# Performance work log

Measured on AMD Instinct MI355X. Metric: run time of the kernel, lower is better.

## Reference

```python
import jax, jax.numpy as jnp
import numpy as np

C = 64
N_H = 4
N_WIN = 16
WIN_L = 8   # compressor window length (overlapped)
WIN_S = 4   # compressor stride -> T//4 blocks


def _rms(x, eps=1e-6):
    return x * jax.lax.rsqrt(jnp.mean(x * x, axis=-1, keepdims=True) + eps)


def _rope(x, negate=False):
    # x: (..., L, D); rotate-half RoPE over positions 0..L-1
    L, D = x.shape[-2], x.shape[-1]
    half = D // 2
    inv_freq = 1.0 / (10000.0 ** (jnp.arange(half, dtype=x.dtype) / half))
    ang = jnp.arange(L, dtype=x.dtype)[:, None] * inv_freq  # (L, half)
    if negate:
        ang = -ang
    cos, sin = jnp.cos(ang), jnp.sin(ang)
    x1, x2 = x[..., :half], x[..., half:]
    return jnp.concatenate([x1 * cos - x2 * sin, x1 * sin + x2 * cos], axis=-1)


def _compress(H, W):
    # overlapped token compressor: windows of WIN_L, stride WIN_S, zero-pad tail
    B, T, d = H.shape
    Tc = T // WIN_S
    Hp = jnp.pad(H, ((0, 0), (0, WIN_L - WIN_S), (0, 0)))
    idx = WIN_S * jnp.arange(Tc)[:, None] + jnp.arange(WIN_L)[None, :]  # (Tc, WIN_L)
    win = Hp[:, idx]                       # (B, Tc, WIN_L, d)
    return win.reshape(B, Tc, WIN_L * d) @ W  # (B, Tc, out)


def setup_inputs() -> dict:
    key = jax.random.key(0)
    ks = jax.random.split(key, 11)
    B, T, d = 2, 2048, 256

    def w(k, shape, fan):
        return jax.random.normal(k, shape, jnp.float32) / np.float32(np.sqrt(fan))

    H = jax.random.normal(ks[0], (B, T, d), jnp.float32)
    return {
        'H': H,
        'Wc_comp': w(ks[1], (WIN_L * d, C), WIN_L * d),
        'Wc_idx': w(ks[2], (WIN_L * d, 32), WIN_L * d),
        'W_DQ': w(ks[3], (d, 64), d),
        'W_IUQ': w(ks[4], (64, 4 * 32), 64),
        'W_w': w(ks[5], (64, 4), 64),
        'W_Q': w(ks[6], (d, N_H * C), d),
        'W_KV': w(ks[7], (d, C), d),
        'g_q': jnp.ones((N_H, C), jnp.float32),
        'g_k': jnp.ones((C,), jnp.float32),
        'g_v': jnp.ones((C,), jnp.float32),
        'Wg0': w(ks[8], (2 * C, 64), 2 * C),
        'bg0': jnp.zeros((64,), jnp.float32),
        'Wg1': w(ks[9], (2 * C, 64), 2 * C),
        'bg1': jnp.zeros((64,), jnp.float32),
        'Wout': w(ks[10], (128, d), 128),
        'bout': jnp.zeros((d,), jnp.float32),
    }


def reference(H, Wc_comp, Wc_idx, W_DQ, W_IUQ, W_w, W_Q, W_KV,
              g_q, g_k, g_v, Wg0, bg0, Wg1, bg1, Wout, bout):
    B, T, d = H.shape
    Tc = T // 4
    k_top = min(8, Tc)

    # ---- lightning indexer ----
    H_dc = H @ W_DQ                                   # (B,T,64)
    Q_I = (H_dc @ W_IUQ).reshape(B, T, 4, 32)         # (B,T,4,32)
    W_Iw = (H_dc @ W_w)[..., None]                    # (B,T,4,1)
    K_I = _compress(H, Wc_idx)                        # (B,Tc,32)
    dot = jnp.einsum('bthc,bsc->bths', Q_I, K_I)      # (B,T,4,Tc)
    I_ts = (W_Iw * jax.nn.relu(dot)).sum(axis=2)      # (B,T,Tc)

    t = jnp.arange(T)[:, None]
    s = jnp.arange(Tc)[None, :]
    mask_I = jnp.where(4 * s <= t, 0.0, -jnp.inf)     # (T,Tc) causal over blocks
    _, topk_idx = jax.lax.top_k(I_ts + mask_I, k_top)  # (B,T,k)
    bI = jnp.arange(B)[:, None, None]
    tI = jnp.arange(T)[None, :, None]
    M_comp = jnp.full((B, T, Tc), -jnp.inf).at[bI, tI, topk_idx].set(0.0)

    # ---- compressed + sliding KV ----
    KV = jnp.concatenate([_compress(H, Wc_comp), H @ W_KV], axis=1)  # (B,Tc+T,C)

    Q = (H @ W_Q).reshape(B, T, N_H, C).transpose(0, 2, 1, 3)        # (B,nh,T,C)
    Q = _rms(Q) * g_q[None, :, None, :]
    K = _rms(KV) * g_k
    V = _rms(KV) * g_v
    Q = _rope(Q)
    K = _rope(K)
    V = _rope(V)

    S = jnp.einsum('bhtc,bsc->bhts', Q, K) / np.float32(np.sqrt(C))  # (B,nh,T,Tc+T)

    S_comp = S[..., :Tc] + M_comp[:, None]
    rel = t - jnp.arange(T)[None, :]
    mask_slide = jnp.where((rel >= 0) & (rel < N_WIN), 0.0, -jnp.inf)  # (T,T)
    S_slide = S[..., Tc:] + mask_slide

    P = jax.nn.softmax(jnp.concatenate([S_comp, S_slide], axis=-1), axis=-1)
    O = jnp.einsum('bhts,bsc->bhtc', P, V)            # (B,nh,T,C)
    O = _rope(O, negate=True)

    O0 = O[:, :2].transpose(0, 2, 1, 3).reshape(B, T, 2 * C)
    O1 = O[:, 2:].transpose(0, 2, 1, 3).reshape(B, T, 2 * C)
    p_all = jnp.concatenate([O0 @ Wg0 + bg0, O1 @ Wg1 + bg1], axis=-1)
    return p_all @ Wout + bout
```

## Files before the change

kernel.cpp:

```cpp
#include <hip/hip_runtime.h>
#include <hip/hip_bf16.h>
#include <math.h>

#define T_DIM 2048
#define B_DIM 2
#define D_DIM 256
#define TC 512
#define KV_LEN 2560

typedef __attribute__((ext_vector_type(8))) short bf16x8;
typedef __attribute__((ext_vector_type(4))) float f32x4;
typedef unsigned short ush;

__device__ __forceinline__ float wave_sum64(float v) {
#pragma unroll
    for (int off = 32; off > 0; off >>= 1) v += __shfl_xor(v, off, 64);
    return v;
}

__device__ __forceinline__ float rope_angle(int pos, int j) {
    float inv = powf(10000.0f, -(float)j * (1.0f / 32.0f));
    return (float)pos * inv;
}

__global__ __launch_bounds__(256) void k_prep(
    const float* __restrict__ H, const float* __restrict__ W_Q,
    const float* __restrict__ W_KV, const float* __restrict__ W_DQ,
    const float* __restrict__ W_IUQ, const float* __restrict__ W_w,
    const float* __restrict__ Wc_comp, const float* __restrict__ Wc_idx,
    const float* __restrict__ Wg0, const float* __restrict__ bg0,
    const float* __restrict__ Wg1, const float* __restrict__ bg1,
    const float* __restrict__ Wout, const float* __restrict__ bout,
    ush* __restrict__ Ap, ush* __restrict__ Ac,
    ush* __restrict__ Bp, ush* __restrict__ Bc,
    ush* __restrict__ Bo, float* __restrict__ biascomb)
{
    int gid = blockIdx.x * 256 + threadIdx.x;
    float vals[8];
    ush* dst;
    bool lo_part;

    if (gid < 262144) {
        int tile = gid >> 10;
        int c = (gid >> 6) & 15;
        int l = gid & 63;
        int bt = tile * 16 + (l & 15);
        int kb = (c & 7) * 32 + (l >> 4) * 8;
        const float* src = H + (size_t)bt * 256 + kb;
#pragma unroll
        for (int j = 0; j < 8; ++j) vals[j] = src[j];
        lo_part = (c >= 8);
        dst = Ap + (size_t)gid * 8;
    } else if (gid < 786432) {
        int g = gid - 262144;
        int tile = g >> 13;
        int c = (g >> 6) & 127;
        int l = g & 63;
        int m = tile * 16 + (l & 15);
        int s = m & 511;
        int b = m >> 9;
        int k2b = (c & 63) * 32 + (l >> 4) * 8;
        int r4 = 4 * s + (k2b >> 8);
        int col = k2b & 255;
        if (r4 < T_DIM) {
            const float* src = H + ((size_t)b * T_DIM + r4) * 256 + col;
#pragma unroll
            for (int j = 0; j < 8; ++j) vals[j] = src[j];
        } else {
#pragma unroll
            for (int j = 0; j < 8; ++j) vals[j] = 0.f;
        }
        lo_part = (c >= 64);
        dst = Ac + (size_t)g * 8;
    } else if (gid < 819200) {
        int g = gid - 786432;
        int tile = g >> 10;
        int c = (g >> 6) & 15;
        int l = g & 63;
        int n = tile * 16 + (l & 15);
        int kb = (c & 7) * 32 + (l >> 4) * 8;
#pragma unroll
        for (int j = 0; j < 8; ++j) {
            int k = kb + j;
            float w;
            if (n < 256)      w = W_Q[(size_t)k * 256 + n];
            else if (n < 320) w = W_KV[(size_t)k * 64 + (n - 256)];
            else if (n < 448) {
                w = 0.f;
                for (int i = 0; i < 64; ++i)
                    w = fmaf(W_DQ[(size_t)k * 64 + i], W_IUQ[(size_t)i * 128 + (n - 320)], w);
            } else if (n < 452) {
                w = 0.f;
                for (int i = 0; i < 64; ++i)
                    w = fmaf(W_DQ[(size_t)k * 64 + i], W_w[(size_t)i * 4 + (n - 448)], w);
            } else {
                w = 0.f;
            }
            vals[j] = w;
        }
        lo_part = (c >= 8);
        dst = Bp + (size_t)g * 8;
    } else if (gid < 868352) {
        int g = gid - 819200;
        int tile = g >> 13;
        int c = (g >> 6) & 127;
        int l = g & 63;
        int n = tile * 16 + (l & 15);
        int k2b = (c & 63) * 32 + (l >> 4) * 8;
#pragma unroll
        for (int j = 0; j < 8; ++j) {
            int k = k2b + j;
            vals[j] = (n < 64) ? Wc_comp[(size_t)k * 64 + n]
                               : Wc_idx[(size_t)k * 32 + (n - 64)];
        }
        lo_part = (c >= 64);
        dst = Bc + (size_t)g * 8;
    } else if (gid < 933888) {
        int g = gid - 868352;
        int k = g >> 8;
        int n = g & 255;
        float acc = 0.f;
        if (k < 128) {
            for (int i = 0; i < 64; ++i)
                acc = fmaf(Wg0[k * 64 + i], Wout[(size_t)i * 256 + n], acc);
        } else {
            for (int i = 0; i < 64; ++i)
                acc = fmaf(Wg1[(k - 128) * 64 + i], Wout[(size_t)(64 + i) * 256 + n], acc);
        }
        __hip_bfloat16 hb = __float2bfloat16(acc);
        float hif = __bfloat162float(hb);
        __hip_bfloat16 lb = __float2bfloat16(acc - hif);
        int tile = n >> 4;
        int chi = k >> 5;
        int lane2 = (n & 15) + 16 * ((k >> 3) & 3);
        int j = k & 7;
        Bo[(size_t)(tile * 16 + chi) * 512 + lane2 * 8 + j] = *(ush*)&hb;
        Bo[(size_t)(tile * 16 + chi + 8) * 512 + lane2 * 8 + j] = *(ush*)&lb;
        return;
    } else if (gid < 934144) {
        int n = gid - 933888;
        float acc = bout[n];
        for (int i = 0; i < 64; ++i) {
            acc = fmaf(bg0[i], Wout[(size_t)i * 256 + n], acc);
            acc = fmaf(bg1[i], Wout[(size_t)(64 + i) * 256 + n], acc);
        }
        biascomb[n] = acc;
        return;
    } else {
        return;
    }

    bf16x8 out8;
#pragma unroll
    for (int j = 0; j < 8; ++j) {
        float x = vals[j];
        __hip_bfloat16 hb = __float2bfloat16(x);
        if (!lo_part) {
            out8[j] = *(short*)&hb;
        } else {
            float hif = __bfloat162float(hb);
            __hip_bfloat16 lb = __float2bfloat16(x - hif);
            out8[j] = *(short*)&lb;
        }
    }
    *(bf16x8*)dst = out8;
}

__global__ __launch_bounds__(64) void k_mfma(
    const ush* __restrict__ Ap, const ush* __restrict__ Ac,
    const ush* __restrict__ Bp, const ush* __restrict__ Bc,
    float* __restrict__ Pre, float* __restrict__ Prec_part)
{
    int lane = threadIdx.x;
    int mrow = lane & 15;
    int q = lane >> 4;

    if (blockIdx.x < 512) {
        int p = blockIdx.x;
        int m0 = (p >> 2) * 32;
        int n0 = (p & 3) * 128;
        int at0 = (m0 >> 4) * 16;
        int bt0n = (n0 >> 4) * 16;

        f32x4 acc[2][8];
#pragma unroll
        for (int mt = 0; mt < 2; ++mt)
#pragma unroll
            for (int nt = 0; nt < 8; ++nt) acc[mt][nt] = (f32x4){0.f, 0.f, 0.f, 0.f};

        for (int c = 0; c < 8; ++c) {
            bf16x8 ahi[2], alo[2], bhi[8], blo[8];
#pragma unroll
            for (int mt = 0; mt < 2; ++mt) {
                ahi[mt] = *(const bf16x8*)(Ap + (size_t)((at0 + mt * 16) + c) * 512 + lane * 8);
                alo[mt] = *(const bf16x8*)(Ap + (size_t)((at0 + mt * 16) + 8 + c) * 512 + lane * 8);
            }
#pragma unroll
            for (int nt = 0; nt < 8; ++nt) {
                bhi[nt] = *(const bf16x8*)(Bp + (size_t)((bt0n + nt * 16) + c) * 512 + lane * 8);
                blo[nt] = *(const bf16x8*)(Bp + (size_t)((bt0n + nt * 16) + 8 + c) * 512 + lane * 8);
            }
#pragma unroll
            for (int mt = 0; mt < 2; ++mt)
#pragma unroll
                for (int nt = 0; nt < 8; ++nt) {
                    acc[mt][nt] = __builtin_amdgcn_mfma_f32_16x16x32_bf16(ahi[mt], bhi[nt], acc[mt][nt], 0, 0, 0);
                    acc[mt][nt] = __builtin_amdgcn_mfma_f32_16x16x32_bf16(ahi[mt], blo[nt], acc[mt][nt], 0, 0, 0);
                    acc[mt][nt] = __builtin_amdgcn_mfma_f32_16x16x32_bf16(alo[mt], bhi[nt], acc[mt][nt], 0, 0, 0);
                }
        }

#pragma unroll
        for (int mt = 0; mt < 2; ++mt)
#pragma unroll
            for (int nt = 0; nt < 8; ++nt)
#pragma unroll
                for (int reg = 0; reg < 4; ++reg)
                    Pre[(size_t)(m0 + 16 * mt + 4 * q + reg) * 512 + n0 + 16 * nt + mrow] =
                        acc[mt][nt][reg];
    } else {
        int cb = blockIdx.x - 512;
        int m0 = (cb >> 2) * 32;
        int q4 = cb & 3;
        int at0 = (m0 >> 4) * 128;

        f32x4 acc[2][6];
#pragma unroll
        for (int mt = 0; mt < 2; ++mt)
#pragma unroll
            for (int nt = 0; nt < 6; ++nt) acc[mt][nt] = (f32x4){0.f, 0.f, 0.f, 0.f};

        for (int cl = 0; cl < 16; ++cl) {
            int c = q4 * 16 + cl;
            bf16x8 ahi[2], alo[2], bhi[6], blo[6];
#pragma unroll
            for (int mt = 0; mt < 2; ++mt) {
                ahi[mt] = *(const bf16x8*)(Ac + (size_t)((at0 + mt * 128) + c) * 512 + lane * 8);
                alo[mt] = *(const bf16x8*)(Ac + (size_t)((at0 + mt * 128) + 64 + c) * 512 + lane * 8);
            }
#pragma unroll
            for (int nt = 0; nt < 6; ++nt) {
                bhi[nt] = *(const bf16x8*)(Bc + (size_t)(nt * 128 + c) * 512 + lane * 8);
                blo[nt] = *(const bf16x8*)(Bc + (size_t)(nt * 128 + 64 + c) * 512 + lane * 8);
            }
#pragma unroll
            for (int mt = 0; mt < 2; ++mt)
#pragma unroll
                for (int nt = 0; nt < 6; ++nt) {
                    acc[mt][nt] = __builtin_amdgcn_mfma_f32_16x16x32_bf16(ahi[mt], bhi[nt], acc[mt][nt], 0, 0, 0);
                    acc[mt][nt] = __builtin_amdgcn_mfma_f32_16x16x32_bf16(ahi[mt], blo[nt], acc[mt][nt], 0, 0, 0);
                    acc[mt][nt] = __builtin_amdgcn_mfma_f32_16x16x32_bf16(alo[mt], bhi[nt], acc[mt][nt], 0, 0, 0);
                }
        }

        float* dst = Prec_part + (size_t)q4 * (1024 * 96);
#pragma unroll
        for (int mt = 0; mt < 2; ++mt)
#pragma unroll
            for (int nt = 0; nt < 6; ++nt)
#pragma unroll
                for (int reg = 0; reg < 4; ++reg)
                    dst[(size_t)(m0 + 16 * mt + 4 * q + reg) * 96 + 16 * nt + mrow] =
                        acc[mt][nt][reg];
    }
}

__global__ __launch_bounds__(256) void k_epi(
    const float* __restrict__ Pre, const float* __restrict__ Prec_part,
    const float* __restrict__ g_q, const float* __restrict__ g_k,
    const float* __restrict__ g_v,
    float* __restrict__ Qr, float* __restrict__ KIbuf,
    float* __restrict__ Kbuf, float* __restrict__ Vbuf)
{
    int tid = threadIdx.x;
    int wv = tid >> 6;
    int lane = tid & 63;

    if (blockIdx.x < 1024) {
        int bt = blockIdx.x * 4 + wv;
        int b = bt >> 11;
        int t = bt & 2047;

        const float* pr = Pre + (size_t)bt * 512;
        int j = lane & 31;
        float s_t, c_t;
        sincosf(rope_angle(t, j), &s_t, &c_t);

#pragma unroll
        for (int r = 0; r < 4; ++r) {
            float qv = pr[r * 64 + lane];
            float ss = wave_sum64(qv * qv);
            float sc = rsqrtf(ss * (1.0f / 64.0f) + 1e-6f);
            float qq = qv * sc * g_q[r * 64 + lane];
            float prt = __shfl_xor(qq, 32, 64);
            float o = (lane < 32) ? fmaf(qq, c_t, -prt * s_t)
                                  : fmaf(prt, s_t, qq * c_t);
            Qr[(size_t)bt * 256 + r * 64 + lane] = o;
        }
        {
            float kvv = pr[256 + lane];
            float ss = wave_sum64(kvv * kvv);
            float sc = rsqrtf(ss * (1.0f / 64.0f) + 1e-6f);
            float kk = kvv * sc * g_k[lane];
            float vv = kvv * sc * g_v[lane];
            int pos = TC + t;
            float s_p, c_p;
            sincosf(rope_angle(pos, j), &s_p, &c_p);
            float pk = __shfl_xor(kk, 32, 64);
            float pv = __shfl_xor(vv, 32, 64);
            float ko = (lane < 32) ? fmaf(kk, c_p, -pk * s_p) : fmaf(pk, s_p, kk * c_p);
            float vo = (lane < 32) ? fmaf(vv, c_p, -pv * s_p) : fmaf(pv, s_p, vv * c_p);
            size_t off = ((size_t)b * KV_LEN + pos) * 64 + lane;
            Kbuf[off] = ko;
            Vbuf[off] = vo;
        }
    } else {
        int sg = (blockIdx.x - 1024) * 4 + wv;
        int b = sg >> 9;
        int s = sg & 511;

        const float* p0 = Prec_part + (size_t)sg * 96;
        float kvv = p0[lane] + p0[98304 + lane] + p0[2 * 98304 + lane] + p0[3 * 98304 + lane];

        float ss = wave_sum64(kvv * kvv);
        float sc = rsqrtf(ss * (1.0f / 64.0f) + 1e-6f);
        float kk = kvv * sc * g_k[lane];
        float vv = kvv * sc * g_v[lane];
        int j = lane & 31;
        float sa, ca;
        sincosf(rope_angle(s, j), &sa, &ca);
        float pk = __shfl_xor(kk, 32, 64);
        float pv = __shfl_xor(vv, 32, 64);
        float ko = (lane < 32) ? fmaf(kk, ca, -pk * sa) : fmaf(pk, sa, kk * ca);
        float vo = (lane < 32) ? fmaf(vv, ca, -pv * sa) : fmaf(pv, sa, vv * ca);
        size_t off = ((size_t)b * KV_LEN + s) * 64 + lane;
        Kbuf[off] = ko;
        Vbuf[off] = vo;

        if (lane < 32) {
            float a = p0[64 + lane] + p0[98304 + 64 + lane] +
                      p0[2 * 98304 + 64 + lane] + p0[3 * 98304 + 64 + lane];
            KIbuf[((size_t)b * TC + s) * 32 + lane] = a;
        }
    }
}

__global__ __launch_bounds__(256) void k_sparse(
    const float* __restrict__ Pre, const float* __restrict__ KIbuf,
    const float* __restrict__ Qr, const float* __restrict__ Kbuf,
    const float* __restrict__ Vbuf, float* __restrict__ Obuf)
{
    int tid = threadIdx.x;
    int wv = tid >> 6;
    int lane = tid & 63;
    int bt0 = blockIdx.x * 4;
    int bt = bt0 + wv;
    int b = bt >> 11;
    int t = bt & 2047;

    __shared__ float sBig[12480];
    __shared__ float sQI[4][128];
    __shared__ float swv[4][4];
    __shared__ float sQr[4][256];
    __shared__ float sP[4][4][24];
    __shared__ int sPos[4][24];

    const float* pr = Pre + (size_t)bt * 512;
    sQI[wv][lane] = pr[320 + lane];
    sQI[wv][64 + lane] = pr[384 + lane];
    if (lane < 4) swv[wv][lane] = pr[448 + lane];

    const float* KIb = KIbuf + (size_t)b * TC * 32;
    int smax = t >> 2;
    int smax_blk = ((bt0 + 3) & 2047) >> 2;

    float vals[8];
#pragma unroll
    for (int r = 0; r < 8; ++r) vals[r] = -INFINITY;

    for (int r = 0; r < 8; ++r) {
        if (r * 64 > smax_blk) break;
        __syncthreads();
        for (int i = tid; i < 512; i += 256) {
            int row = i >> 3;
            int cseg = (i & 7) * 4;
            float4 v = *(const float4*)(KIb + (size_t)(r * 64 + row) * 32 + cseg);
            float* dstp = &sBig[row * 33 + cseg];
            dstp[0] = v.x; dstp[1] = v.y; dstp[2] = v.z; dstp[3] = v.w;
        }
        __syncthreads();

        int s = r * 64 + lane;
        if (s <= smax) {
            float dd0 = 0.f, dd1 = 0.f, dd2 = 0.f, dd3 = 0.f;
#pragma unroll
            for (int c = 0; c < 32; ++c) {
                float kv = sBig[lane * 33 + c];
                dd0 = fmaf(sQI[wv][c], kv, dd0);
                dd1 = fmaf(sQI[wv][32 + c], kv, dd1);
                dd2 = fmaf(sQI[wv][64 + c], kv, dd2);
                dd3 = fmaf(sQI[wv][96 + c], kv, dd3);
            }
            vals[r] = swv[wv][0] * fmaxf(dd0, 0.f) + swv[wv][1] * fmaxf(dd1, 0.f) +
                      swv[wv][2] * fmaxf(dd2, 0.f) + swv[wv][3] * fmaxf(dd3, 0.f);
        }
    }

    unsigned consumed = 0u;
    for (int k2 = 0; k2 < 8; ++k2) {
        float bv = -INFINITY;
        int bi = 0x7fffffff;
#pragma unroll
        for (int r = 0; r < 8; ++r) {
            if (!(consumed & (1u << r))) {
                int s = lane + 64 * r;
                float v = vals[r];
                if (v > bv || (v == bv && s < bi)) { bv = v; bi = s; }
            }
        }
#pragma unroll
        for (int off = 1; off < 64; off <<= 1) {
            float ov = __shfl_xor(bv, off, 64);
            int oi = __shfl_xor(bi, off, 64);
            if (ov > bv || (ov == bv && oi < bi)) { bv = ov; bi = oi; }
        }
        if ((bi & 63) == lane) consumed |= 1u << (bi >> 6);
        if (lane == 0) sPos[wv][k2] = bi;
    }
    if (lane >= 8 && lane < 24) {
        int rel = lane - 8;
        int sp = t - rel;
        sPos[wv][lane] = (sp >= 0) ? (TC + sp) : -1;
    }
    __syncthreads();

    float (*sKV)[48 * 65] = (float (*)[48 * 65])sBig;
#pragma unroll
    for (int lt = 0; lt < 4; ++lt) {
        for (int i = tid; i < 768; i += 256) {
            int row = i >> 4;
            int seg = (i & 15) << 2;
            int key = (row < 24) ? row : row - 24;
            int pos = sPos[lt][key];
            if (pos >= 0) {
                const float* src = ((row < 24) ? Kbuf : Vbuf) +
                                   ((size_t)b * KV_LEN + pos) * 64 + seg;
                float4 v = *(const float4*)src;
                float* dstp = &sKV[lt][row * 65 + seg];
                dstp[0] = v.x; dstp[1] = v.y; dstp[2] = v.z; dstp[3] = v.w;
            }
        }
    }
    for (int i = tid; i < 1024; i += 256)
        sQr[i >> 8][i & 255] = Qr[(size_t)(bt0 + (i >> 8)) * 256 + (i & 255)];
    __syncthreads();

    int j = lane & 31;
    float sa, ca;
    sincosf(rope_angle(t, j), &sa, &ca);

#pragma unroll
    for (int h = 0; h < 4; ++h) {
        float scv = -INFINITY;
        if (lane < 24) {
            int pos = sPos[wv][lane];
            if (pos >= 0) {
                float dd = 0.f;
#pragma unroll
                for (int c = 0; c < 64; ++c)
                    dd = fmaf(sQr[wv][h * 64 + c], sKV[wv][lane * 65 + c], dd);
                scv = dd * 0.125f;
            }
        }
        float m = scv;
#pragma unroll
        for (int off = 1; off < 64; off <<= 1) m = fmaxf(m, __shfl_xor(m, off, 64));
        float p = expf(scv - m);
        if (scv == -INFINITY) p = 0.f;
        float l = p;
#pragma unroll
        for (int off = 1; off < 64; off <<= 1) l += __shfl_xor(l, off, 64);
        p /= l;
        if (lane < 24) sP[wv][h][lane] = p;

        float o = 0.f;
#pragma unroll
        for (int j2 = 0; j2 < 24; ++j2) {
            int pos = sPos[wv][j2];
            if (pos >= 0)
                o = fmaf(sP[wv][h][j2], sKV[wv][(24 + j2) * 65 + lane], o);
        }

        float prt = __shfl_xor(o, 32, 64);
        float oo = (lane < 32) ? fmaf(o, ca, prt * sa) : fmaf(-prt, sa, o * ca);
        Obuf[(size_t)bt * 256 + h * 64 + lane] = oo;
    }
}

__global__ __launch_bounds__(64) void k_out(
    const float* __restrict__ Obuf, const ush* __restrict__ Bo,
    const float* __restrict__ biascomb, float* __restrict__ out)
{
    int lane = threadIdx.x;
    int mrow = lane & 15;
    int q = lane >> 4;
    int p = blockIdx.x;
    int m0 = (p >> 2) * 32;
    int n0 = (p & 3) * 64;
    int bt0n = (n0 >> 4) * 16;

    f32x4 acc[2][4];
#pragma unroll
    for (int mt = 0; mt < 2; ++mt)
#pragma unroll
        for (int nt = 0; nt < 4; ++nt) acc[mt][nt] = (f32x4){0.f, 0.f, 0.f, 0.f};

    for (int c = 0; c < 8; ++c) {
        bf16x8 ahi[2], alo[2], bhi[4], blo[4];
#pragma unroll
        for (int mt = 0; mt < 2; ++mt) {
            const float* src = Obuf + (size_t)(m0 + 16 * mt + mrow) * 256 + c * 32 + 8 * q;
            float4 x0 = *(const float4*)src;
            float4 x1 = *(const float4*)(src + 4);
            float xs[8] = {x0.x, x0.y, x0.z, x0.w, x1.x, x1.y, x1.z, x1.w};
#pragma unroll
            for (int j = 0; j < 8; ++j) {
                __hip_bfloat16 hb = __float2bfloat16(xs[j]);
                float hif = __bfloat162float(hb);
                __hip_bfloat16 lb = __float2bfloat16(xs[j] - hif);
                ahi[mt][j] = *(short*)&hb;
                alo[mt][j] = *(short*)&lb;
            }
        }
#pragma unroll
        for (int nt = 0; nt < 4; ++nt) {
            bhi[nt] = *(const bf16x8*)(Bo + (size_t)((bt0n + nt * 16) + c) * 512 + lane * 8);
            blo[nt] = *(const bf16x8*)(Bo + (size_t)((bt0n + nt * 16) + 8 + c) * 512 + lane * 8);
        }
#pragma unroll
        for (int mt = 0; mt < 2; ++mt)
#pragma unroll
            for (int nt = 0; nt < 4; ++nt) {
                acc[mt][nt] = __builtin_amdgcn_mfma_f32_16x16x32_bf16(ahi[mt], bhi[nt], acc[mt][nt], 0, 0, 0);
                acc[mt][nt] = __builtin_amdgcn_mfma_f32_16x16x32_bf16(ahi[mt], blo[nt], acc[mt][nt], 0, 0, 0);
                acc[mt][nt] = __builtin_amdgcn_mfma_f32_16x16x32_bf16(alo[mt], bhi[nt], acc[mt][nt], 0, 0, 0);
            }
    }

#pragma unroll
    for (int mt = 0; mt < 2; ++mt)
#pragma unroll
        for (int nt = 0; nt < 4; ++nt) {
            float bia = biascomb[n0 + 16 * nt + mrow];
#pragma unroll
            for (int reg = 0; reg < 4; ++reg)
                out[(size_t)(m0 + 16 * mt + 4 * q + reg) * 256 + n0 + 16 * nt + mrow] =
                    acc[mt][nt][reg] + bia;
        }
}

extern "C" void kernel_launch(void* const* d_in, const int* in_sizes, int n_in,
                              void* d_out, int out_size, void* d_ws, size_t ws_size,
                              hipStream_t stream) {
    const float* H       = (const float*)d_in[0];
    const float* Wc_comp = (const float*)d_in[1];
    const float* Wc_idx  = (const float*)d_in[2];
    const float* W_DQ    = (const float*)d_in[3];
    const float* W_IUQ   = (const float*)d_in[4];
    const float* W_w     = (const float*)d_in[5];
    const float* W_Q     = (const float*)d_in[6];
    const float* W_KV    = (const float*)d_in[7];
    const float* g_q     = (const float*)d_in[8];
    const float* g_k     = (const float*)d_in[9];
    const float* g_v     = (const float*)d_in[10];
    const float* Wg0     = (const float*)d_in[11];
    const float* bg0     = (const float*)d_in[12];
    const float* Wg1     = (const float*)d_in[13];
    const float* bg1     = (const float*)d_in[14];
    const float* Wout    = (const float*)d_in[15];
    const float* bout    = (const float*)d_in[16];

    float* ws = (float*)d_ws;
    float* Qr   = ws;
    float* KI   = ws + 1048576;
    float* Kb   = ws + 1081344;
    float* Vb   = ws + 1409024;
    float* Pre  = ws + 1736704;
    float* Prec = ws + 3833856;
    float* Obuf = ws + 4227072;
    ush* Ap = (ush*)(ws + 5275648);
    ush* Ac = (ush*)(ws + 6324224);
    ush* Bp = (ush*)(ws + 8421376);
    ush* Bc = (ush*)(ws + 8552448);
    ush* Bo = (ush*)(ws + 8749056);
    float* biascomb = ws + 8814592;

    float* outp = (float*)d_out;

    hipLaunchKernelGGL(k_prep, dim3(3649), dim3(256), 0, stream,
                       H, W_Q, W_KV, W_DQ, W_IUQ, W_w, Wc_comp, Wc_idx,
                       Wg0, bg0, Wg1, bg1, Wout, bout,
                       Ap, Ac, Bp, Bc, Bo, biascomb);
    hipLaunchKernelGGL(k_mfma, dim3(640), dim3(64), 0, stream,
                       Ap, Ac, Bp, Bc, Pre, Prec);
    hipLaunchKernelGGL(k_epi, dim3(1280), dim3(256), 0, stream,
                       Pre, Prec, g_q, g_k, g_v, Qr, KI, Kb, Vb);
    hipLaunchKernelGGL(k_sparse, dim3(1024), dim3(256), 0, stream,
                       Pre, KI, Qr, Kb, Vb, Obuf);
    hipLaunchKernelGGL(k_out, dim3(512), dim3(64), 0, stream,
                       Obuf, Bo, biascomb, outp);
}
```

Before: 204.5 us.

## Split sparse attention into top-k scoring and per-head attention kernels

The fused sparse kernel is split into a score/top-k kernel that writes the selected indices to a workspace buffer, and a separate attention kernel with 1024 threads per block that handles each head in its own wave instead of looping over heads serially. The aim is to cut shared-memory pressure in the scoring kernel for better occupancy, and to spread the four heads across waves for more parallelism. The cost is an extra launch and a global round trip for the top-k indices. The large shared footprint of 1024-thread blocks may also limit residency.

```diff
diff --git a/kernel.cpp b/kernel.cpp
--- a/kernel.cpp
+++ b/kernel.cpp
@@ -345,10 +345,9 @@
     }
 }
 
-__global__ __launch_bounds__(256) void k_sparse(
+__global__ __launch_bounds__(256) void k_score_topk(
     const float* __restrict__ Pre, const float* __restrict__ KIbuf,
-    const float* __restrict__ Qr, const float* __restrict__ Kbuf,
-    const float* __restrict__ Vbuf, float* __restrict__ Obuf)
+    int* __restrict__ topk)
 {
     int tid = threadIdx.x;
     int wv = tid >> 6;
@@ -358,17 +357,14 @@
     int b = bt >> 11;
     int t = bt & 2047;
 
-    __shared__ float sBig[12480];
-    __shared__ float sQI[4][128];
-    __shared__ float swv[4][4];
-    __shared__ float sQr[4][256];
-    __shared__ float sP[4][4][24];
-    __shared__ int sPos[4][24];
+    __shared__ float sQ[4][128];
+    __shared__ float sw[4][4];
+    __shared__ float sKI[64 * 33];
 
     const float* pr = Pre + (size_t)bt * 512;
-    sQI[wv][lane] = pr[320 + lane];
-    sQI[wv][64 + lane] = pr[384 + lane];
-    if (lane < 4) swv[wv][lane] = pr[448 + lane];
+    sQ[wv][lane] = pr[320 + lane];
+    sQ[wv][64 + lane] = pr[384 + lane];
+    if (lane < 4) sw[wv][lane] = pr[448 + lane];
 
     const float* KIb = KIbuf + (size_t)b * TC * 32;
     int smax = t >> 2;
@@ -385,7 +381,7 @@
             int row = i >> 3;
             int cseg = (i & 7) * 4;
             float4 v = *(const float4*)(KIb + (size_t)(r * 64 + row) * 32 + cseg);
-            float* dstp = &sBig[row * 33 + cseg];
+            float* dstp = &sKI[row * 33 + cseg];
             dstp[0] = v.x; dstp[1] = v.y; dstp[2] = v.z; dstp[3] = v.w;
         }
         __syncthreads();
@@ -395,14 +391,14 @@
             float dd0 = 0.f, dd1 = 0.f, dd2 = 0.f, dd3 = 0.f;
 #pragma unroll
             for (int c = 0; c < 32; ++c) {
-                float kv = sBig[lane * 33 + c];
-                dd0 = fmaf(sQI[wv][c], kv, dd0);
-                dd1 = fmaf(sQI[wv][32 + c], kv, dd1);
-                dd2 = fmaf(sQI[wv][64 + c], kv, dd2);
-                dd3 = fmaf(sQI[wv][96 + c], kv, dd3);
-            }
-            vals[r] = swv[wv][0] * fmaxf(dd0, 0.f) + swv[wv][1] * fmaxf(dd1, 0.f) +
-                      swv[wv][2] * fmaxf(dd2, 0.f) + swv[wv][3] * fmaxf(dd3, 0.f);
+                float kv = sKI[lane * 33 + c];
+                dd0 = fmaf(sQ[wv][c], kv, dd0);
+                dd1 = fmaf(sQ[wv][32 + c], kv, dd1);
+                dd2 = fmaf(sQ[wv][64 + c], kv, dd2);
+                dd3 = fmaf(sQ[wv][96 + c], kv, dd3);
+            }
+            vals[r] = sw[wv][0] * fmaxf(dd0, 0.f) + sw[wv][1] * fmaxf(dd1, 0.f) +
+                      sw[wv][2] * fmaxf(dd2, 0.f) + sw[wv][3] * fmaxf(dd3, 0.f);
         }
     }
 
@@ -425,76 +421,90 @@
             if (ov > bv || (ov == bv && oi < bi)) { bv = ov; bi = oi; }
         }
         if ((bi & 63) == lane) consumed |= 1u << (bi >> 6);
-        if (lane == 0) sPos[wv][k2] = bi;
-    }
-    if (lane >= 8 && lane < 24) {
-        int rel = lane - 8;
+        if (lane == 0) topk[(size_t)bt * 8 + k2] = bi;
+    }
+}
+
+__global__ __launch_bounds__(1024) void k_attn(
+    const float* __restrict__ Qr, const float* __restrict__ Kbuf,
+    const float* __restrict__ Vbuf, const int* __restrict__ topk,
+    float* __restrict__ Obuf)
+{
+    int tid = threadIdx.x;
+    int lt = tid >> 8;
+    int t256 = tid & 255;
+    int h = t256 >> 6;
+    int lane = tid & 63;
+    int bt = blockIdx.x * 4 + lt;
+    int b = bt >> 11;
+    int t = bt & 2047;
+
+    __shared__ float sKV[4][48 * 65];
+    __shared__ float sQ[4][256];
+    __shared__ int sPos[4][24];
+    __shared__ float sP[4][4][24];
+
+    sQ[lt][t256] = Qr[(size_t)bt * 256 + t256];
+    if (t256 < 8) {
+        sPos[lt][t256] = topk[(size_t)bt * 8 + t256];
+    } else if (t256 < 24) {
+        int rel = t256 - 8;
         int sp = t - rel;
-        sPos[wv][lane] = (sp >= 0) ? (TC + sp) : -1;
+        sPos[lt][t256] = (sp >= 0) ? (TC + sp) : -1;
     }
     __syncthreads();
 
-    float (*sKV)[48 * 65] = (float (*)[48 * 65])sBig;
-#pragma unroll
-    for (int lt = 0; lt < 4; ++lt) {
-        for (int i = tid; i < 768; i += 256) {
-            int row = i >> 4;
-            int seg = (i & 15) << 2;
-            int key = (row < 24) ? row : row - 24;
-            int pos = sPos[lt][key];
-            if (pos >= 0) {
-                const float* src = ((row < 24) ? Kbuf : Vbuf) +
-                                   ((size_t)b * KV_LEN + pos) * 64 + seg;
-                float4 v = *(const float4*)src;
-                float* dstp = &sKV[lt][row * 65 + seg];
-                dstp[0] = v.x; dstp[1] = v.y; dstp[2] = v.z; dstp[3] = v.w;
-            }
-        }
-    }
-    for (int i = tid; i < 1024; i += 256)
-        sQr[i >> 8][i & 255] = Qr[(size_t)(bt0 + (i >> 8)) * 256 + (i & 255)];
+    for (int i = t256; i < 768; i += 256) {
+        int row = i >> 4;
+        int seg = (i & 15) << 2;
+        int key = (row < 24) ? row : row - 24;
+        int pos = sPos[lt][key];
+        if (pos >= 0) {
+            const float* src = ((row < 24) ? Kbuf : Vbuf) +
+                               ((size_t)b * KV_LEN + pos) * 64 + seg;
+            float4 v = *(const float4*)src;
+            float* dst = &sKV[lt][row * 65 + seg];
+            dst[0] = v.x; dst[1] = v.y; dst[2] = v.z; dst[3] = v.w;
+        }
+    }
     __syncthreads();
+
+    float scv = -INFINITY;
+    if (lane < 24) {
+        int pos = sPos[lt][lane];
+        if (pos >= 0) {
+            float dd = 0.f;
+#pragma unroll
+            for (int c = 0; c < 64; ++c)
+                dd = fmaf(sQ[lt][h * 64 + c], sKV[lt][lane * 65 + c], dd);
+            scv = dd * 0.125f;
+        }
+    }
+    float m = scv;
+#pragma unroll
+    for (int off = 1; off < 64; off <<= 1) m = fmaxf(m, __shfl_xor(m, off, 64));
+    float p = expf(scv - m);
+    if (scv == -INFINITY) p = 0.f;
+    float l = p;
+#pragma unroll
+    for (int off = 1; off < 64; off <<= 1) l += __shfl_xor(l, off, 64);
+    p /= l;
+    if (lane < 24) sP[lt][h][lane] = p;
+
+    float o = 0.f;
+#pragma unroll
+    for (int j2 = 0; j2 < 24; ++j2) {
+        int pos = sPos[lt][j2];
+        if (pos >= 0)
+            o = fmaf(sP[lt][h][j2], sKV[lt][(24 + j2) * 65 + lane], o);
+    }
 
     int j = lane & 31;
     float sa, ca;
     sincosf(rope_angle(t, j), &sa, &ca);
-
-#pragma unroll
-    for (int h = 0; h < 4; ++h) {
-        float scv = -INFINITY;
-        if (lane < 24) {
-            int pos = sPos[wv][lane];
-            if (pos >= 0) {
-                float dd = 0.f;
-#pragma unroll
-                for (int c = 0; c < 64; ++c)
-                    dd = fmaf(sQr[wv][h * 64 + c], sKV[wv][lane * 65 + c], dd);
-                scv = dd * 0.125f;
-            }
-        }
-        float m = scv;
-#pragma unroll
-        for (int off = 1; off < 64; off <<= 1) m = fmaxf(m, __shfl_xor(m, off, 64));
-        float p = expf(scv - m);
-        if (scv == -INFINITY) p = 0.f;
-        float l = p;
-#pragma unroll
-        for (int off = 1; off < 64; off <<= 1) l += __shfl_xor(l, off, 64);
-        p /= l;
-        if (lane < 24) sP[wv][h][lane] = p;
-
-        float o = 0.f;
-#pragma unroll
-        for (int j2 = 0; j2 < 24; ++j2) {
-            int pos = sPos[wv][j2];
-            if (pos >= 0)
-                o = fmaf(sP[wv][h][j2], sKV[wv][(24 + j2) * 65 + lane], o);
-        }
-
-        float prt = __shfl_xor(o, 32, 64);
-        float oo = (lane < 32) ? fmaf(o, ca, prt * sa) : fmaf(-prt, sa, o * ca);
-        Obuf[(size_t)bt * 256 + h * 64 + lane] = oo;
-    }
+    float prt = __shfl_xor(o, 32, 64);
+    float oo = (lane < 32) ? fmaf(o, ca, prt * sa) : fmaf(-prt, sa, o * ca);
+    Obuf[(size_t)bt * 256 + h * 64 + lane] = oo;
 }
 
 __global__ __launch_bounds__(64) void k_out(
@@ -588,12 +598,13 @@
     float* Pre  = ws + 1736704;
     float* Prec = ws + 3833856;
     float* Obuf = ws + 4227072;
-    ush* Ap = (ush*)(ws + 5275648);
-    ush* Ac = (ush*)(ws + 6324224);
-    ush* Bp = (ush*)(ws + 8421376);
-    ush* Bc = (ush*)(ws + 8552448);
-    ush* Bo = (ush*)(ws + 8749056);
-    float* biascomb = ws + 8814592;
+    int* topkb  = (int*)(ws + 5275648);
+    ush* Ap = (ush*)(ws + 5308416);
+    ush* Ac = (ush*)(ws + 6356992);
+    ush* Bp = (ush*)(ws + 8454144);
+    ush* Bc = (ush*)(ws + 8585216);
+    ush* Bo = (ush*)(ws + 8781824);
+    float* biascomb = ws + 8847360;
 
     float* outp = (float*)d_out;
 
@@ -605,8 +616,10 @@
                        Ap, Ac, Bp, Bc, Pre, Prec);
     hipLaunchKernelGGL(k_epi, dim3(1280), dim3(256), 0, stream,
                        Pre, Prec, g_q, g_k, g_v, Qr, KI, Kb, Vb);
-    hipLaunchKernelGGL(k_sparse, dim3(1024), dim3(256), 0, stream,
-                       Pre, KI, Qr, Kb, Vb, Obuf);
+    hipLaunchKernelGGL(k_score_topk, dim3(1024), dim3(256), 0, stream,
+                       Pre, KI, topkb);
+    hipLaunchKernelGGL(k_attn, dim3(1024), dim3(1024), 0, stream,
+                       Qr, Kb, Vb, topkb, Obuf);
     hipLaunchKernelGGL(k_out, dim3(512), dim3(64), 0, stream,
                        Obuf, Bo, biascomb, outp);
 }
```

After: 176.6 us. 1.16x faster.
